# Optimization experiments

Hardware: AMD Instinct MI355X
Metric: run time of the kernel (lower is better)

## Reference

```python
import jax, jax.numpy as jnp
import numpy as np
from jax import lax

N, L, V, ES, HS = 16384, 512, 32000, 32, 64


def setup_inputs() -> dict:
    key = jax.random.key(0)
    k_tok, k_len, k_emb, k_wih, k_whh, k_bih, k_bhh = jax.random.split(key, 7)
    # valid tokens in [1, V) so that (x != 0).sum(1) == true prefix length
    tok = jax.random.randint(k_tok, (N, L), 1, V)
    lengths = jax.random.randint(k_len, (N,), 0, L + 1)  # includes empty seqs
    x = jnp.where(jnp.arange(L)[None, :] < lengths[:, None], tok, 0)
    s = 0.1
    embedding = jax.random.normal(k_emb, (V, ES), dtype=jnp.float32) * s
    w_ih = jax.random.normal(k_wih, (3 * HS, ES), dtype=jnp.float32) * s  # [r|z|n] stacked (torch order)
    w_hh = jax.random.normal(k_whh, (3 * HS, HS), dtype=jnp.float32) * s
    b_ih = jax.random.normal(k_bih, (3 * HS,), dtype=jnp.float32) * s
    b_hh = jax.random.normal(k_bhh, (3 * HS,), dtype=jnp.float32) * s
    return {"x": x, "embedding": embedding, "w_ih": w_ih, "w_hh": w_hh,
            "b_ih": b_ih, "b_hh": b_hh}


def reference(x, embedding, w_ih, w_hh, b_ih, b_hh):
    # Faithful math: final GRU hidden state over the nonzero prefix of each row;
    # rows with length 0 return zeros (h0). Equivalent to bucketed
    # pack_padded_sequence + GRU + scatter of final hidden states.
    n, l = x.shape
    hs = w_hh.shape[1]
    lengths = (x != 0).sum(axis=1)  # [n]

    def step(h, inp):
        t, xt = inp                      # xt: [n] token ids at time t
        e = embedding[xt]                # [n, es] gather
        gx = e @ w_ih.T + b_ih           # [n, 3*hs]
        gh = h @ w_hh.T + b_hh           # [n, 3*hs]
        xr, xz, xn = jnp.split(gx, 3, axis=-1)
        hr, hz, hn = jnp.split(gh, 3, axis=-1)
        r = jax.nn.sigmoid(xr + hr)
        z = jax.nn.sigmoid(xz + hz)
        ng = jnp.tanh(xn + r * hn)
        h_new = (1.0 - z) * ng + z * h   # torch GRU update
        h = jnp.where((t < lengths)[:, None], h_new, h)  # freeze past length
        return h, None

    h0 = jnp.zeros((n, hs), dtype=embedding.dtype)
    hT, _ = lax.scan(step, h0, (jnp.arange(l), x.T))
    return hT
```

## Files before the change

kernel.cpp:

```cpp
#include <hip/hip_runtime.h>

#define N_SEQ 16384
#define LSEQ  512
#define VOCAB 32000
#define ES    32
#define HS    64
#define LDH   72
#define TS    18

#define SC_RZ (-1.4426950408889634f)
#define SC_N  (-2.8853900817779268f)

typedef _Float16 v8h __attribute__((ext_vector_type(8)));
typedef float    v4f __attribute__((ext_vector_type(4)));

#define NLB (N_SEQ / 256)
#define NEB (VOCAB * ES / 256)
__global__ __launch_bounds__(256) void k_prep(const int* __restrict__ x,
                                              const float* __restrict__ emb,
                                              const float* __restrict__ whh,
                                              const float* __restrict__ wih,
                                              int* __restrict__ len,
                                              int* __restrict__ hist,
                                              _Float16* __restrict__ ef,
                                              _Float16* __restrict__ wpk,
                                              _Float16* __restrict__ wpe){
  int b = blockIdx.x;
  if (b < NLB){
    int row = b * 256 + threadIdx.x;
    const int* xr = x + (size_t)row * LSEQ;
    int lo = 0, hi = LSEQ;
    while (lo < hi){ int mid = (lo + hi) >> 1; if (xr[mid] != 0) lo = mid + 1; else hi = mid; }
    len[row] = lo;
    atomicAdd(&hist[lo], 1);
  } else if (b < NLB + NEB){
    int i = (b - NLB) * 256 + threadIdx.x;
    ef[i] = (_Float16)emb[i];
  } else if (b < NLB + NEB + 6){
    int tid = (b - NLB - NEB) * 256 + threadIdx.x;
    int f = tid >> 6, l = tid & 63;
    int jt = f >> 1, kf = f & 1;
    float sc = (jt < 8) ? SC_RZ : SC_N;
    #pragma unroll
    for (int i = 0; i < 8; ++i){
      int row = jt * 16 + (l & 15);
      int col = kf * 32 + (l >> 4) * 8 + i;
      wpk[(size_t)tid * 8 + i] = (_Float16)(sc * whh[row * HS + col]);
    }
  } else {
    int tid = (b - NLB - NEB - 6) * 256 + threadIdx.x;
    int tile = tid >> 6, l = tid & 63;
    float sc = ((tile >> 2) < 2) ? SC_RZ : SC_N;
    #pragma unroll
    for (int i = 0; i < 8; ++i){
      int row = tile * 16 + (l & 15);
      int col = (l >> 4) * 8 + i;
      wpe[(size_t)tid * 8 + i] = (_Float16)(sc * wih[row * ES + col]);
    }
  }
}

__global__ __launch_bounds__(1024) void k_scatter(const int* __restrict__ hist,
                                                  const int* __restrict__ len,
                                                  int* __restrict__ gcnt,
                                                  int* __restrict__ perm){
  __shared__ int buf[1024];
  __shared__ int offs[513];
  int i = threadIdx.x;
  buf[i] = (i < 513) ? hist[i] : 0;
  __syncthreads();
  for (int d = 1; d < 1024; d <<= 1){
    int v = (i >= d) ? buf[i - d] : 0;
    __syncthreads();
    buf[i] += v;
    __syncthreads();
  }
  if (i < 513) offs[i] = (i == 0) ? 0 : buf[i - 1];
  __syncthreads();
  int s = blockIdx.x * 1024 + i;
  int l = len[s];
  int pos = offs[l] + atomicAdd(&gcnt[l], 1);
  perm[pos] = s;
}

__global__ __launch_bounds__(256, 4) void k_gru(
    const int* __restrict__ x, const _Float16* __restrict__ ef,
    const _Float16* __restrict__ wpk, const _Float16* __restrict__ wpe,
    const float* __restrict__ bih, const float* __restrict__ bhh,
    const int* __restrict__ perm, const int* __restrict__ len,
    float* __restrict__ out)
{
  __shared__ __align__(16) _Float16 hb[2][16 * LDH];
  __shared__ unsigned short tok[(LSEQ + 2) * TS];
  int qt   = threadIdx.x >> 6;
  int w = blockIdx.x >> 8, cq = blockIdx.x & 255;
  int rank = w * 256 + ((w & 1) ? (255 - cq) : cq);
  int grp  = 1023 - rank;
  int lane = threadIdx.x & 63;
  int q = lane >> 4, c = lane & 15;
  int uu = qt*16 + c;

  v8h bfh[3][2], bfe[3];
  #pragma unroll
  for (int g = 0; g < 3; ++g){
    int tile = g*4 + qt;
    #pragma unroll
    for (int kf = 0; kf < 2; ++kf)
      bfh[g][kf] = *(const v8h*)(wpk + ((size_t)(tile*2 + kf)*64 + lane)*8);
    bfe[g] = *(const v8h*)(wpe + ((size_t)tile*64 + lane)*8);
  }

  int sq[4], ln[4];
  #pragma unroll
  for (int r = 0; r < 4; ++r){
    int s = perm[grp * 16 + q*4 + r];
    sq[r] = s;
    ln[r] = len[s];
  }
  float br  = SC_RZ * (bih[uu]      + bhh[uu]);
  float bz  = SC_RZ * (bih[HS + uu] + bhh[HS + uu]);
  float ben = SC_N  *  bih[2*HS + uu];
  float bhn = SC_N  *  bhh[2*HS + uu];
  v4f brq  = {br, br, br, br};
  v4f bzq  = {bz, bz, bz, bz};
  v4f benq = {ben, ben, ben, ben};
  v4f bhnq = {bhn, bhn, bhn, bhn};

  float h[4];
  #pragma unroll
  for (int r = 0; r < 4; ++r) h[r] = 0.f;

  for (int i = threadIdx.x; i < 16*LDH; i += 256) hb[0][i] = (_Float16)0.f;

  for (int j = threadIdx.x; j < 16*LSEQ; j += 256){
    int s = j >> 9, tt = j & (LSEQ-1);
    tok[tt*TS + s] = (unsigned short)x[(size_t)perm[grp*16 + s] * LSEQ + tt];
  }
  if (threadIdx.x < 32){
    tok[(LSEQ + (threadIdx.x >> 4))*TS + (threadIdx.x & 15)] = 0;
  }
  __syncthreads();

  int tmax = max(max(ln[0], ln[1]), max(ln[2], ln[3]));
  tmax = max(tmax, __shfl_xor(tmax, 16, 64));
  tmax = max(tmax, __shfl_xor(tmax, 32, 64));
  int tmin = min(min(ln[0], ln[1]), min(ln[2], ln[3]));
  tmin = min(tmin, __shfl_xor(tmin, 16, 64));
  tmin = min(tmin, __shfl_xor(tmin, 32, 64));

  v8h aec, aen;
  v4f pra, prb, pza, pzb, dea, deb;
  {
    int tk0 = tok[0*TS + c];
    aec = *(const v8h*)(ef + (size_t)tk0 * ES + q*8);
    pra = __builtin_amdgcn_mfma_f32_16x16x32_f16(aec, bfe[0], brq,  0,0,0);
    pza = __builtin_amdgcn_mfma_f32_16x16x32_f16(aec, bfe[1], bzq,  0,0,0);
    dea = __builtin_amdgcn_mfma_f32_16x16x32_f16(aec, bfe[2], benq, 0,0,0);
    int tk1 = tok[1*TS + c];
    aen = *(const v8h*)(ef + (size_t)tk1 * ES + q*8);
  }

  #define GRU_STEP(FREEZE, ACONS, ALOAD, PRR, PRZ, DEN, PRRn, PRZn, DENn, RB, WB) \
  {                                                                            \
    int tkn = tok[(t + 2)*TS + c];                                             \
    v8h a0 = *(const v8h*)(&hb[RB][c*LDH + q*8]);                              \
    v8h a1 = *(const v8h*)(&hb[RB][c*LDH + 32 + q*8]);                         \
    v4f zr  = __builtin_amdgcn_mfma_f32_16x16x32_f16(a1, bfh[0][1], PRR, 0,0,0);\
    v4f Dr  = __builtin_amdgcn_mfma_f32_16x16x32_f16(a0, bfh[0][0], zr,  0,0,0);\
    v4f zz  = __builtin_amdgcn_mfma_f32_16x16x32_f16(a1, bfh[1][1], PRZ, 0,0,0);\
    v4f Dz  = __builtin_amdgcn_mfma_f32_16x16x32_f16(a0, bfh[1][0], zz,  0,0,0);\
    v4f zh  = __builtin_amdgcn_mfma_f32_16x16x32_f16(a1, bfh[2][1], bhnq,0,0,0);\
    v4f Dhn = __builtin_amdgcn_mfma_f32_16x16x32_f16(a0, bfh[2][0], zh,  0,0,0);\
    _Pragma("unroll")                                                          \
    for (int r = 0; r < 4; ++r){                                               \
      float rg   = __builtin_amdgcn_rcpf(1.f + __builtin_amdgcn_exp2f(Dr[r])); \
      float zg   = __builtin_amdgcn_rcpf(1.f + __builtin_amdgcn_exp2f(Dz[r])); \
      float te   = __builtin_amdgcn_exp2f(DEN[r] + rg * Dhn[r]);               \
      float ng   = fmaf(2.f, __builtin_amdgcn_rcpf(1.f + te), -1.f);           \
      float hnew = ng + zg * (h[r] - ng);                                      \
      h[r]       = (FREEZE && t >= ln[r]) ? h[r] : hnew;                       \
    }                                                                          \
    PRRn = __builtin_amdgcn_mfma_f32_16x16x32_f16(ACONS, bfe[0], brq,  0,0,0); \
    PRZn = __builtin_amdgcn_mfma_f32_16x16x32_f16(ACONS, bfe[1], bzq,  0,0,0); \
    DENn = __builtin_amdgcn_mfma_f32_16x16x32_f16(ACONS, bfe[2], benq, 0,0,0); \
    ALOAD = *(const v8h*)(ef + (size_t)tkn * ES + q*8);           \
    _Pragma("unroll")                                                          \
    for (int r = 0; r < 4; ++r)                                                \
      hb[WB][(q*4 + r)*LDH + uu] = (_Float16)h[r];                             \
    asm volatile("s_waitcnt lgkmcnt(0)" ::: "memory");                         \
    __builtin_amdgcn_s_barrier();                                              \
    asm volatile("" ::: "memory");                                             \
  }

  int t = 0;
  for (; t + 1 < tmin; ){
    GRU_STEP(0, aen, aec, pra, pza, dea, prb, pzb, deb, 0, 1); ++t;
    GRU_STEP(0, aec, aen, prb, pzb, deb, pra, pza, dea, 1, 0); ++t;
  }
  for (; t + 1 < tmax; ){
    GRU_STEP(1, aen, aec, pra, pza, dea, prb, pzb, deb, 0, 1); ++t;
    GRU_STEP(1, aec, aen, prb, pzb, deb, pra, pza, dea, 1, 0); ++t;
  }
  if (t < tmax){
    GRU_STEP(1, aen, aec, pra, pza, dea, prb, pzb, deb, 0, 1); ++t;
  }
  #undef GRU_STEP

  #pragma unroll
  for (int r = 0; r < 4; ++r)
    out[(size_t)sq[r] * HS + uu] = h[r];
}

extern "C" void kernel_launch(void* const* d_in, const int* in_sizes, int n_in,
                              void* d_out, int out_size, void* d_ws, size_t ws_size,
                              hipStream_t stream){
  const int*   x   = (const int*)  d_in[0];
  const float* emb = (const float*)d_in[1];
  const float* wih = (const float*)d_in[2];
  const float* whh = (const float*)d_in[3];
  const float* bih = (const float*)d_in[4];
  const float* bhh = (const float*)d_in[5];
  float* out = (float*)d_out;

  char* ws = (char*)d_ws;
  size_t off = 0;
  _Float16* ef  = (_Float16*)(ws + off);  off += (size_t)VOCAB * ES * sizeof(_Float16);
  _Float16* wpk = (_Float16*)(ws + off);  off += (size_t)24 * 64 * 8 * sizeof(_Float16);
  _Float16* wpe = (_Float16*)(ws + off);  off += (size_t)12 * 64 * 8 * sizeof(_Float16);
  off = (off + 255) & ~(size_t)255;
  int* len  = (int*)(ws + off);           off += (size_t)N_SEQ * sizeof(int);
  int* perm = (int*)(ws + off);           off += (size_t)N_SEQ * sizeof(int);
  int* hist = (int*)(ws + off);           off += 513 * sizeof(int);
  int* gcnt = (int*)(ws + off);           off += 513 * sizeof(int);

  hipMemsetAsync(hist, 0, 2 * 513 * sizeof(int), stream);
  k_prep   <<<NLB + NEB + 9, 256, 0, stream>>>(x, emb, whh, wih, len, hist, ef, wpk, wpe);
  k_scatter<<<N_SEQ / 1024, 1024, 0, stream>>>(hist, len, gcnt, perm);
  k_gru    <<<N_SEQ / 16,    256, 0, stream>>>(x, ef, wpk, wpe, bih, bhh, perm, len, out);
}
```

Baseline: 309.9 us.

## Break MFMA accumulation chain, store hidden earlier, vectorize prep kernel

Each gate's two K-half MFMAs in the recurrent step no longer chain through the accumulator. The second now starts from zero and the two results are added with vector adds, which shortens the dependent MFMA latency per step. The fp16 hidden-state writes to LDS move ahead of the next-step input-projection MFMAs, so the LDS stores can overlap that work before the barrier. Separately, the prep kernel counts lengths with one wavefront per row and vectorized loads plus a shuffle reduction instead of a per-thread binary search, and converts the embedding table eight elements per thread.

```diff
diff --git a/kernel.cpp b/kernel.cpp
--- a/kernel.cpp
+++ b/kernel.cpp
@@ -14,8 +14,8 @@
 typedef _Float16 v8h __attribute__((ext_vector_type(8)));
 typedef float    v4f __attribute__((ext_vector_type(4)));
 
-#define NLB (N_SEQ / 256)
-#define NEB (VOCAB * ES / 256)
+#define NLB (N_SEQ / 4)
+#define NEB (VOCAB * ES / 2048)
 __global__ __launch_bounds__(256) void k_prep(const int* __restrict__ x,
                                               const float* __restrict__ emb,
                                               const float* __restrict__ whh,
@@ -27,35 +27,50 @@
                                               _Float16* __restrict__ wpe){
   int b = blockIdx.x;
   if (b < NLB){
-    int row = b * 256 + threadIdx.x;
-    const int* xr = x + (size_t)row * LSEQ;
-    int lo = 0, hi = LSEQ;
-    while (lo < hi){ int mid = (lo + hi) >> 1; if (xr[mid] != 0) lo = mid + 1; else hi = mid; }
-    len[row] = lo;
-    atomicAdd(&hist[lo], 1);
+    int row  = b * 4 + (threadIdx.x >> 6);
+    int lane = threadIdx.x & 63;
+    const int4* xr = (const int4*)(x + (size_t)row * LSEQ);
+    int cnt = 0;
+    #pragma unroll
+    for (int i = 0; i < 2; ++i){
+      int4 v = xr[lane + i*64];
+      cnt += (v.x != 0) + (v.y != 0) + (v.z != 0) + (v.w != 0);
+    }
+    #pragma unroll
+    for (int d = 1; d < 64; d <<= 1) cnt += __shfl_xor(cnt, d, 64);
+    if (lane == 0){ len[row] = cnt; atomicAdd(&hist[cnt], 1); }
   } else if (b < NLB + NEB){
-    int i = (b - NLB) * 256 + threadIdx.x;
-    ef[i] = (_Float16)emb[i];
-  } else if (b < NLB + NEB + 6){
+    int i = ((b - NLB) * 256 + threadIdx.x) * 8;
+    float4 f0 = *(const float4*)(emb + i);
+    float4 f1 = *(const float4*)(emb + i + 4);
+    v8h o;
+    o[0] = (_Float16)f0.x; o[1] = (_Float16)f0.y;
+    o[2] = (_Float16)f0.z; o[3] = (_Float16)f0.w;
+    o[4] = (_Float16)f1.x; o[5] = (_Float16)f1.y;
+    o[6] = (_Float16)f1.z; o[7] = (_Float16)f1.w;
+    *(v8h*)(ef + i) = o;
+  } else {
     int tid = (b - NLB - NEB) * 256 + threadIdx.x;
-    int f = tid >> 6, l = tid & 63;
-    int jt = f >> 1, kf = f & 1;
-    float sc = (jt < 8) ? SC_RZ : SC_N;
-    #pragma unroll
-    for (int i = 0; i < 8; ++i){
-      int row = jt * 16 + (l & 15);
-      int col = kf * 32 + (l >> 4) * 8 + i;
-      wpk[(size_t)tid * 8 + i] = (_Float16)(sc * whh[row * HS + col]);
-    }
-  } else {
-    int tid = (b - NLB - NEB - 6) * 256 + threadIdx.x;
-    int tile = tid >> 6, l = tid & 63;
-    float sc = ((tile >> 2) < 2) ? SC_RZ : SC_N;
-    #pragma unroll
-    for (int i = 0; i < 8; ++i){
-      int row = tile * 16 + (l & 15);
-      int col = (l >> 4) * 8 + i;
-      wpe[(size_t)tid * 8 + i] = (_Float16)(sc * wih[row * ES + col]);
+    if (tid < 1536){
+      int f = tid >> 6, l = tid & 63;
+      int jt = f >> 1, kf = f & 1;
+      float sc = (jt < 8) ? SC_RZ : SC_N;
+      #pragma unroll
+      for (int i = 0; i < 8; ++i){
+        int row = jt * 16 + (l & 15);
+        int col = kf * 32 + (l >> 4) * 8 + i;
+        wpk[(size_t)tid * 8 + i] = (_Float16)(sc * whh[row * HS + col]);
+      }
+    } else if (tid < 1536 + 768){
+      int t2 = tid - 1536;
+      int tile = t2 >> 6, l = t2 & 63;
+      float sc = ((tile >> 2) < 2) ? SC_RZ : SC_N;
+      #pragma unroll
+      for (int i = 0; i < 8; ++i){
+        int row = tile * 16 + (l & 15);
+        int col = (l >> 4) * 8 + i;
+        wpe[(size_t)t2 * 8 + i] = (_Float16)(sc * wih[row * ES + col]);
+      }
     }
   }
 }
@@ -125,6 +140,7 @@
   v4f bzq  = {bz, bz, bz, bz};
   v4f benq = {ben, ben, ben, ben};
   v4f bhnq = {bhn, bhn, bhn, bhn};
+  const v4f zero4 = {0.f, 0.f, 0.f, 0.f};
 
   float h[4];
   #pragma unroll
@@ -165,12 +181,15 @@
     int tkn = tok[(t + 2)*TS + c];                                             \
     v8h a0 = *(const v8h*)(&hb[RB][c*LDH + q*8]);                              \
     v8h a1 = *(const v8h*)(&hb[RB][c*LDH + 32 + q*8]);                         \
-    v4f zr  = __builtin_amdgcn_mfma_f32_16x16x32_f16(a1, bfh[0][1], PRR, 0,0,0);\
-    v4f Dr  = __builtin_amdgcn_mfma_f32_16x16x32_f16(a0, bfh[0][0], zr,  0,0,0);\
-    v4f zz  = __builtin_amdgcn_mfma_f32_16x16x32_f16(a1, bfh[1][1], PRZ, 0,0,0);\
-    v4f Dz  = __builtin_amdgcn_mfma_f32_16x16x32_f16(a0, bfh[1][0], zz,  0,0,0);\
-    v4f zh  = __builtin_amdgcn_mfma_f32_16x16x32_f16(a1, bfh[2][1], bhnq,0,0,0);\
-    v4f Dhn = __builtin_amdgcn_mfma_f32_16x16x32_f16(a0, bfh[2][0], zh,  0,0,0);\
+    v4f ur  = __builtin_amdgcn_mfma_f32_16x16x32_f16(a1, bfh[0][1], PRR, 0,0,0);\
+    v4f vr  = __builtin_amdgcn_mfma_f32_16x16x32_f16(a0, bfh[0][0], zero4,0,0,0);\
+    v4f uz  = __builtin_amdgcn_mfma_f32_16x16x32_f16(a1, bfh[1][1], PRZ, 0,0,0);\
+    v4f vz  = __builtin_amdgcn_mfma_f32_16x16x32_f16(a0, bfh[1][0], zero4,0,0,0);\
+    v4f uh  = __builtin_amdgcn_mfma_f32_16x16x32_f16(a1, bfh[2][1], bhnq,0,0,0);\
+    v4f vh  = __builtin_amdgcn_mfma_f32_16x16x32_f16(a0, bfh[2][0], zero4,0,0,0);\
+    v4f Dr  = ur + vr;                                                         \
+    v4f Dz  = uz + vz;                                                         \
+    v4f Dhn = uh + vh;                                                         \
     _Pragma("unroll")                                                          \
     for (int r = 0; r < 4; ++r){                                               \
       float rg   = __builtin_amdgcn_rcpf(1.f + __builtin_amdgcn_exp2f(Dr[r])); \
@@ -180,13 +199,13 @@
       float hnew = ng + zg * (h[r] - ng);                                      \
       h[r]       = (FREEZE && t >= ln[r]) ? h[r] : hnew;                       \
     }                                                                          \
+    _Pragma("unroll")                                                          \
+    for (int r = 0; r < 4; ++r)                                                \
+      hb[WB][(q*4 + r)*LDH + uu] = (_Float16)h[r];                             \
     PRRn = __builtin_amdgcn_mfma_f32_16x16x32_f16(ACONS, bfe[0], brq,  0,0,0); \
     PRZn = __builtin_amdgcn_mfma_f32_16x16x32_f16(ACONS, bfe[1], bzq,  0,0,0); \
     DENn = __builtin_amdgcn_mfma_f32_16x16x32_f16(ACONS, bfe[2], benq, 0,0,0); \
     ALOAD = *(const v8h*)(ef + (size_t)tkn * ES + q*8);           \
-    _Pragma("unroll")                                                          \
-    for (int r = 0; r < 4; ++r)                                                \
-      hb[WB][(q*4 + r)*LDH + uu] = (_Float16)h[r];                             \
     asm volatile("s_waitcnt lgkmcnt(0)" ::: "memory");                         \
     __builtin_amdgcn_s_barrier();                                              \
     asm volatile("" ::: "memory");                                             \
```

Measured after the change: 322.5 us. 4.0% more time.
